# Kernel optimization log

Hardware: AMD Instinct MI355X
Metric: run time of the kernel (lower is better)

Reference implementation:

```python
import jax, jax.numpy as jnp
import numpy as np

# ExLoss constants (use_prior=False path)
T = 10.0
W_BU, W_H, W_TH = 1.0, 1.0, 3.0
P_MARGIN, N_MARGIN = 0.2, 0.3

B, C, D = 32, 40000, 2048


def setup_inputs() -> dict:
    key = jax.random.key(0)
    k1, k2, k3, k4 = jax.random.split(key, 4)
    inputs = jax.random.normal(k1, (B, D), dtype=jnp.float32)
    targets = jax.random.randint(k2, (B,), 0, 16)            # few identities -> positive pairs exist
    indexs = jax.random.randint(k3, (B,), 0, C)              # unused (use_prior=False)
    label_to_pairs = jnp.zeros((B,), dtype=jnp.int32)        # unused placeholder
    V = jax.random.normal(k4, (C, D), dtype=jnp.float32)
    V = V / jnp.linalg.norm(V, axis=1, keepdims=True)        # bank rows are L2-normalized by the EMA update
    return {"inputs": inputs, "V": V, "targets": targets,
            "label_to_pairs": label_to_pairs, "indexs": indexs}


def _masked_bce(logits, mask, target):
    # BCEWithLogits, reduction='mean' over masked elements; 0 if mask empty
    # per-elem: target*softplus(-x) + (1-target)*softplus(x)
    per = target * jax.nn.softplus(-logits) + (1.0 - target) * jax.nn.softplus(logits)
    cnt = jnp.sum(mask)
    s = jnp.sum(jnp.where(mask, per, 0.0))
    return jnp.where(cnt > 0, s / jnp.maximum(cnt, 1), 0.0)


def _ex_loss(inputs, V, targets):
    n = inputs.shape[0]
    # Exclusive: memory-bank matmul, scaled by t
    outputs = (inputs @ V.T) * T                                   # [B, C]
    # bu_loss: cross entropy (mean)
    logp = jax.nn.log_softmax(outputs, axis=1)
    bu_loss = -jnp.mean(jnp.take_along_axis(logp, targets[:, None], axis=1))

    # hard_negative_mining (batch sims, off-diagonal)
    ni = inputs / jnp.linalg.norm(inputs, axis=1, keepdims=True)
    sims = ni @ ni.T                                               # [B, B]
    eye = jnp.eye(n, dtype=bool)
    same = targets[:, None] == targets[None, :]
    pos = same & ~eye                                              # positive pairs, diag removed
    neg = ~same                                                    # negatives (diag is always 'same')
    # n_thrds: row min of psims BEFORE 2->-2 replacement (fill=2 where not positive)
    n_thrds = jnp.min(jnp.where(pos, sims, 2.0), axis=1, keepdims=True) - N_MARGIN
    # p_thrds: row max after 2->-2 replacement (fill=-2 where not positive)
    p_thrds = jnp.max(jnp.where(pos, sims, -2.0), axis=1, keepdims=True) - P_MARGIN
    hp_mask = pos & (sims < p_thrds)        # fill value 2 can never be < p_thrds (<= 0.8)
    hn_mask = neg & (sims > n_thrds)        # fill value -2 can never be > n_thrds
    h_loss = _masked_bce(sims, hp_mask, 1.0) + _masked_bce(sims, hn_mask, 0.0)

    # hard_negative_mining_with_table (only if no zero rows in V)
    active = jnp.all(jnp.sum(V, axis=1) != 0)
    nV = ni @ V.T                                                  # [B, C]
    n_th_t = jnp.take_along_axis(nV, targets[:, None], axis=1) - N_MARGIN  # [B,1]
    nsims_t = V[targets] @ V.T                                     # [B, C]
    t_mask = (n_th_t < nsims_t) & (nsims_t < 0.9999)
    th_loss = jnp.where(active, _masked_bce(nsims_t, t_mask, 0.0), 0.0)

    loss = W_BU * bu_loss + W_H * h_loss + W_TH * th_loss
    return loss, outputs


def reference(inputs, V, targets, label_to_pairs, indexs):
    # label_to_pairs / indexs unused: use_prior=False in ExLoss.__init__
    return _ex_loss(inputs, V, targets)
```

## Files before the change

### kernel.cpp

```cpp
#include <hip/hip_runtime.h>
#include <math.h>

#define B_ 32
#define C_ 40000
#define D_ 2048
#define T_SCALE 10.0f
#define P_MARG 0.2f
#define N_MARG 0.3f
#define NSTEP 64
#define KSPL 4
#define NCB 625
#define NBLK (NCB * KSPL)

typedef __attribute__((ext_vector_type(4))) float f32x4;
typedef __fp16 fp16x2 __attribute__((ext_vector_type(2)));
typedef _Float16 f16x2n __attribute__((ext_vector_type(2)));
typedef _Float16 half8_t __attribute__((ext_vector_type(8)));

#define OP1_OFF 0
#define OP_FLOATS (B_ * C_)
#define NS0_OFF (OP1_OFF + 3 * OP_FLOATS)
#define VR_OFF (NS0_OFF + 4 * OP_FLOATS)
#define VR_FLOATS C_
#define SC_OFF (VR_OFF + VR_FLOATS)
#define S_HLOSS 0
#define S_THSUM 1
#define S_THCNT 2
#define S_BAD 3
#define S_NTH 4
#define S_BU 36
#define SC_FLOATS 128
#define DT_OFF (SC_OFF + SC_FLOATS)
#define DT_FLOATS (32 * 32)
#define AF_OFF (DT_OFF + DT_FLOATS)
#define AF_FLOATS (NSTEP * 2048 / 2)
#define WS_FLOATS_TOTAL (AF_OFF + AF_FLOATS)

__device__ __forceinline__ float softplus_f(float x) {
    return (x > 0.f) ? (x + log1pf(expf(-x))) : log1pf(expf(x));
}

__device__ __forceinline__ unsigned pack_rtz(float x0, float x1) {
    fp16x2 h = __builtin_amdgcn_cvt_pkrtz(x0, x1);
    return __builtin_bit_cast(unsigned, h);
}

__device__ __forceinline__ unsigned pack_rtne(float x0, float x1) {
    f16x2n p = {(_Float16)x0, (_Float16)x1};
    return __builtin_bit_cast(unsigned, p);
}

__global__ __launch_bounds__(256) void build_Afrag(const float* __restrict__ in,
                                                   const float* __restrict__ V,
                                                   const int* __restrict__ tgt,
                                                   unsigned short* __restrict__ Af) {
    int s = blockIdx.x;
    int f = threadIdx.x >> 6;
    int l = threadIdx.x & 63;
    int row = f * 16 + (l & 15);
    int k = s * 32 + (l >> 4) * 8;
    const float* src = (row < 32) ? (in + (size_t)row * D_ + k)
                                  : (V + (size_t)tgt[row - 32] * D_ + k);
    f32x4 x0 = *(const f32x4*)src;
    f32x4 x1 = *(const f32x4*)(src + 4);
    uint4 u = make_uint4(pack_rtne(x0[0], x0[1]), pack_rtne(x0[2], x0[3]),
                         pack_rtne(x1[0], x1[1]), pack_rtne(x1[2], x1[3]));
    *(uint4*)(Af + (size_t)s * 2048 + (size_t)f * 512 + (size_t)l * 8) = u;
}

__global__ __launch_bounds__(256) void sims_dots(const float* __restrict__ in,
                                                 float* __restrict__ dt) {
    __shared__ float part[8][32];
    int i = blockIdx.x;
    int j = threadIdx.x & 31;
    int sl = threadIdx.x >> 5;
    const float4* a4 = (const float4*)(in + (size_t)i * D_ + sl * 256);
    const float4* b4 = (const float4*)(in + (size_t)j * D_ + sl * 256);
    float s = 0.f;
#pragma unroll 4
    for (int k = 0; k < 64; ++k) {
        float4 x = a4[k], y = b4[k];
        s += x.x * y.x + x.y * y.y + x.z * y.z + x.w * y.w;
    }
    part[sl][j] = s;
    __syncthreads();
    if (threadIdx.x < 32) {
        float t = 0.f;
#pragma unroll
        for (int p = 0; p < 8; ++p) t += part[p][threadIdx.x];
        dt[i * 32 + threadIdx.x] = t;
    }
}

__global__ __launch_bounds__(1024) void small_finish(const float* __restrict__ in,
                                                     const float* __restrict__ V,
                                                     const int* __restrict__ tgt,
                                                     float* __restrict__ ws) {
    __shared__ float sims[32][33];
    __shared__ float nthr[32], pthr[32];
    __shared__ int ts[32];
    __shared__ float diag[32];
    __shared__ float red[4];
    int tid = threadIdx.x;
    int i = tid >> 5, j = tid & 31;
    const float* dt = ws + DT_OFF;
    if (tid < 32) { ts[tid] = tgt[tid]; diag[tid] = dt[tid * 32 + tid]; }
    if (tid < 4) red[tid] = 0.f;
    __syncthreads();
    float sim = dt[i * 32 + j] * rsqrtf(diag[i] * diag[j]);
    sims[i][j] = sim;
    __syncthreads();
    if (tid < 32) {
        float nmin = 2.f, pmax = -2.f;
        int ti = ts[tid];
        for (int jj = 0; jj < 32; ++jj) {
            bool pos = (ts[jj] == ti) && (jj != tid);
            float v = sims[tid][jj];
            if (pos) { nmin = fminf(nmin, v); pmax = fmaxf(pmax, v); }
        }
        nthr[tid] = nmin - N_MARG;
        pthr[tid] = pmax - P_MARG;
    }
    __syncthreads();
    bool pos = (ts[i] == ts[j]) && (i != j);
    bool neg = (ts[i] != ts[j]);
    if (pos && sim < pthr[i]) { atomicAdd(&red[0], softplus_f(-sim)); atomicAdd(&red[1], 1.f); }
    if (neg && sim > nthr[i]) { atomicAdd(&red[2], softplus_f(sim)); atomicAdd(&red[3], 1.f); }

    const float4* a4 = (const float4*)(in + (size_t)i * D_);
    const float4* v4 = (const float4*)(V + (size_t)ts[i] * D_);
    float sn = 0.f;
    for (int k = j; k < D_ / 4; k += 32) {
        float4 x = a4[k], y = v4[k];
        sn += x.x * y.x + x.y * y.y + x.z * y.z + x.w * y.w;
    }
    for (int off = 16; off > 0; off >>= 1) sn += __shfl_down(sn, off, 32);
    if (j == 0) ws[SC_OFF + S_NTH + i] = sn * rsqrtf(diag[i]) - N_MARG;
    __syncthreads();
    if (tid == 0) {
        float h = 0.f;
        if (red[1] > 0.f) h += red[0] / red[1];
        if (red[3] > 0.f) h += red[2] / red[3];
        ws[SC_OFF + S_HLOSS] = h;
    }
}

__global__ __launch_bounds__(256, 2) void gemm_mfma(const float* __restrict__ V,
                                                    const unsigned short* __restrict__ Af,
                                                    float* __restrict__ op0,
                                                    float* __restrict__ ws) {
    const int l = threadIdx.x & 63;
    const int w = threadIdx.x >> 6;
    const int ks = blockIdx.x & 3;
    const int cb = blockIdx.x >> 2;
    const int col = l & 15, g = l >> 4;
    const int c = cb * 64 + w * 16 + col;

    const float* vp = V + (size_t)c * D_ + ks * 512 + g * 8;
    const unsigned short* ap = Af + (size_t)(ks * 16) * 2048 + (size_t)l * 8;

    f32x4 z = {0.f, 0.f, 0.f, 0.f};
    f32x4 acc0 = z, acc1 = z, acc2 = z, acc3 = z;
    float vsum = 0.f;

    uint4 Aa[4][4], Ab[4][4];
    f32x4 VaA[4], VbA[4], VaB[4], VbB[4];

#define LOADB(AB, VA, VB, t0)                                      \
    _Pragma("unroll") for (int s = 0; s < 4; ++s) {                \
        const unsigned short* as = ap + (size_t)((t0) + s) * 2048; \
        AB[s][0] = *(const uint4*)(as + 0 * 512);                  \
        AB[s][1] = *(const uint4*)(as + 1 * 512);                  \
        AB[s][2] = *(const uint4*)(as + 2 * 512);                  \
        AB[s][3] = *(const uint4*)(as + 3 * 512);                  \
        VA[s] = *(const f32x4*)(vp + ((t0) + s) * 32);             \
        VB[s] = *(const f32x4*)(vp + ((t0) + s) * 32 + 4);         \
    }

#define COMPB(AB, VA, VB)                                                          \
    _Pragma("unroll") for (int s = 0; s < 4; ++s) {                                \
        f32x4 v0 = VA[s], v1 = VB[s];                                              \
        vsum += v0[0] + v0[1] + v0[2] + v0[3] + v1[0] + v1[1] + v1[2] + v1[3];     \
        uint4 bu = make_uint4(pack_rtz(v0[0], v0[1]), pack_rtz(v0[2], v0[3]),      \
                              pack_rtz(v1[0], v1[1]), pack_rtz(v1[2], v1[3]));     \
        half8_t bh = __builtin_bit_cast(half8_t, bu);                              \
        half8_t A0h = __builtin_bit_cast(half8_t, AB[s][0]);                       \
        half8_t A1h = __builtin_bit_cast(half8_t, AB[s][1]);                       \
        half8_t A2h = __builtin_bit_cast(half8_t, AB[s][2]);                       \
        half8_t A3h = __builtin_bit_cast(half8_t, AB[s][3]);                       \
        acc0 = __builtin_amdgcn_mfma_f32_16x16x32_f16(A0h, bh, acc0, 0, 0, 0);     \
        acc1 = __builtin_amdgcn_mfma_f32_16x16x32_f16(A1h, bh, acc1, 0, 0, 0);     \
        acc2 = __builtin_amdgcn_mfma_f32_16x16x32_f16(A2h, bh, acc2, 0, 0, 0);     \
        acc3 = __builtin_amdgcn_mfma_f32_16x16x32_f16(A3h, bh, acc3, 0, 0, 0);     \
    }

    LOADB(Aa, VaA, VbA, 0);
    LOADB(Ab, VaB, VbB, 4);
    COMPB(Aa, VaA, VbA);
    LOADB(Aa, VaA, VbA, 8);
    COMPB(Ab, VaB, VbB);
    LOADB(Ab, VaB, VbB, 12);
    COMPB(Aa, VaA, VbA);
    COMPB(Ab, VaB, VbB);

#undef LOADB
#undef COMPB

    vsum += __shfl_xor(vsum, 16);
    vsum += __shfl_xor(vsum, 32);
    if (g == 0) atomicAdd(&ws[VR_OFF + c], vsum);

    float* op = (ks == 0) ? op0 : (ws + OP1_OFF + (size_t)(ks - 1) * OP_FLOATS);
    float* nsp = ws + NS0_OFF + (size_t)ks * OP_FLOATS;
#pragma unroll
    for (int r = 0; r < 4; ++r) {
        int rr = g * 4 + r;
        op[(size_t)rr * C_ + c] = acc0[r];
        op[(size_t)(16 + rr) * C_ + c] = acc1[r];
        nsp[(size_t)rr * C_ + c] = acc2[r];
        nsp[(size_t)(16 + rr) * C_ + c] = acc3[r];
    }
}

__global__ __launch_bounds__(1024) void lse_th_combine(float* __restrict__ out,
                                                       const int* __restrict__ tgt,
                                                       float* __restrict__ ws) {
    int b = blockIdx.x;
    int tid = threadIdx.x;
    __shared__ float sm[1024], ss[1024], sts[1024], stc[1024];
    __shared__ float xt;
    const float* p1 = ws + OP1_OFF + 0 * OP_FLOATS + (size_t)b * C_;
    const float* p2 = ws + OP1_OFF + 1 * OP_FLOATS + (size_t)b * C_;
    const float* p3 = ws + OP1_OFF + 2 * OP_FLOATS + (size_t)b * C_;
    const float* q0 = ws + NS0_OFF + 0 * OP_FLOATS + (size_t)b * C_;
    const float* q1 = ws + NS0_OFF + 1 * OP_FLOATS + (size_t)b * C_;
    const float* q2 = ws + NS0_OFF + 2 * OP_FLOATS + (size_t)b * C_;
    const float* q3 = ws + NS0_OFF + 3 * OP_FLOATS + (size_t)b * C_;
    float* orow = out + (size_t)b * C_;
    float nth = ws[SC_OFF + S_NTH + b];
    int tg = tgt[b];
    float m = -INFINITY, s = 0.f, ts = 0.f, tc = 0.f;
    for (int c = tid; c < C_; c += 1024) {
        float x = (orow[c] + p1[c] + p2[c] + p3[c]) * T_SCALE;
        orow[c] = x;
        if (c == tg) xt = x;
        float mn = fmaxf(m, x);
        s = s * expf(m - mn) + expf(x - mn);
        m = mn;
        float q = q0[c] + q1[c] + q2[c] + q3[c];
        if (q > nth && q < 0.9999f) { ts += softplus_f(q); tc += 1.f; }
    }
    sm[tid] = m; ss[tid] = s; sts[tid] = ts; stc[tid] = tc;
    __syncthreads();
    for (int st2 = 512; st2 > 0; st2 >>= 1) {
        if (tid < st2) {
            float m2 = sm[tid + st2], s2 = ss[tid + st2];
            float M = fmaxf(sm[tid], m2);
            ss[tid] = ss[tid] * expf(sm[tid] - M) + s2 * expf(m2 - M);
            sm[tid] = M;
            sts[tid] += sts[tid + st2];
            stc[tid] += stc[tid + st2];
        }
        __syncthreads();
    }
    if (tid == 0) {
        ws[SC_OFF + S_BU + b] = (sm[0] + logf(ss[0])) - xt;
        if (stc[0] != 0.f) {
            atomicAdd(&ws[SC_OFF + S_THSUM], sts[0]);
            atomicAdd(&ws[SC_OFF + S_THCNT], stc[0]);
        }
    }
}

__global__ __launch_bounds__(256) void vrow_check(const float* __restrict__ ws_c,
                                                  float* __restrict__ ws) {
    int c = blockIdx.x * 256 + threadIdx.x;
    if (c < C_ && ws_c[VR_OFF + c] == 0.0f) ws[SC_OFF + S_BAD] = 1.0f;
}

__global__ void finalize(const float* __restrict__ ws, float* __restrict__ out0) {
    if (threadIdx.x == 0 && blockIdx.x == 0) {
        float bu = 0.f;
        for (int b = 0; b < 32; ++b) bu += ws[SC_OFF + S_BU + b];
        bu /= 32.f;
        float h = ws[SC_OFF + S_HLOSS];
        float th = 0.f;
        float cnt = ws[SC_OFF + S_THCNT];
        if (ws[SC_OFF + S_BAD] == 0.f && cnt > 0.f) th = ws[SC_OFF + S_THSUM] / cnt;
        out0[0] = 1.0f * bu + 1.0f * h + 3.0f * th;
    }
}

extern "C" void kernel_launch(void* const* d_in, const int* in_sizes, int n_in,
                              void* d_out, int out_size, void* d_ws, size_t ws_size,
                              hipStream_t stream) {
    const float* in = (const float*)d_in[0];
    const float* V = (const float*)d_in[1];
    const int* tgt = (const int*)d_in[2];
    float* outp = (float*)d_out;
    float* ws = (float*)d_ws;
    unsigned short* Af = (unsigned short*)(ws + AF_OFF);

    (void)hipMemsetAsync((void*)(ws + VR_OFF), 0,
                         (size_t)(VR_FLOATS + SC_FLOATS) * sizeof(float), stream);

    build_Afrag<<<NSTEP, 256, 0, stream>>>(in, V, tgt, Af);
    sims_dots<<<32, 256, 0, stream>>>(in, ws + DT_OFF);
    small_finish<<<1, 1024, 0, stream>>>(in, V, tgt, ws);

    gemm_mfma<<<NBLK, 256, 0, stream>>>(V, Af, outp + 1, ws);

    lse_th_combine<<<B_, 1024, 0, stream>>>(outp + 1, tgt, ws);
    vrow_check<<<(C_ + 255) / 256, 256, 0, stream>>>(ws, ws);
    finalize<<<1, 64, 0, stream>>>(ws, outp);
}
```

Baseline: 220.9 us.

## Stage V tiles into LDS via global_load_lds with swizzled double buffering

The GEMM kernel now copies V rows into a double-buffered, XOR-swizzled shared-memory tile with direct global-to-LDS loads, so each row is fetched as contiguous 512-byte chunks rather than strided per-lane 32-byte reads. The A fragments are loaded straight from global memory inside the compute loop instead of being prefetched into registers. This is meant to improve coalescing of the dominant V stream and to cut register pressure. In exchange it adds 64KB of LDS per block and block-wide barriers, which may lower occupancy, and A-load latency is no longer hidden by explicit prefetch.

```diff
diff --git a/kernel.cpp b/kernel.cpp
--- a/kernel.cpp
+++ b/kernel.cpp
@@ -16,6 +16,11 @@
 typedef __fp16 fp16x2 __attribute__((ext_vector_type(2)));
 typedef _Float16 f16x2n __attribute__((ext_vector_type(2)));
 typedef _Float16 half8_t __attribute__((ext_vector_type(8)));
+
+#define GLL(gsrc, ldst)                                                          \
+    __builtin_amdgcn_global_load_lds(                                            \
+        (const __attribute__((address_space(1))) unsigned int*)(gsrc),           \
+        (__attribute__((address_space(3))) unsigned int*)(ldst), 16, 0, 0)
 
 #define OP1_OFF 0
 #define OP_FLOATS (B_ * C_)
@@ -149,62 +154,73 @@
                                                     const unsigned short* __restrict__ Af,
                                                     float* __restrict__ op0,
                                                     float* __restrict__ ws) {
+    __shared__ float Va[4][16][128];
+    __shared__ float Vb[4][16][128];
     const int l = threadIdx.x & 63;
     const int w = threadIdx.x >> 6;
     const int ks = blockIdx.x & 3;
     const int cb = blockIdx.x >> 2;
     const int col = l & 15, g = l >> 4;
-    const int c = cb * 64 + w * 16 + col;
-
-    const float* vp = V + (size_t)c * D_ + ks * 512 + g * 8;
-    const unsigned short* ap = Af + (size_t)(ks * 16) * 2048 + (size_t)l * 8;
+    const int crow0 = cb * 64 + w * 16;
+    const int c = crow0 + col;
+    const int lhi = l >> 5;
+    const int l31 = l & 31;
+    const int c7 = col & 7;
 
     f32x4 z = {0.f, 0.f, 0.f, 0.f};
     f32x4 acc0 = z, acc1 = z, acc2 = z, acc3 = z;
     float vsum = 0.f;
 
-    uint4 Aa[4][4], Ab[4][4];
-    f32x4 VaA[4], VbA[4], VaB[4], VbB[4];
-
-#define LOADB(AB, VA, VB, t0)                                      \
-    _Pragma("unroll") for (int s = 0; s < 4; ++s) {                \
-        const unsigned short* as = ap + (size_t)((t0) + s) * 2048; \
-        AB[s][0] = *(const uint4*)(as + 0 * 512);                  \
-        AB[s][1] = *(const uint4*)(as + 1 * 512);                  \
-        AB[s][2] = *(const uint4*)(as + 2 * 512);                  \
-        AB[s][3] = *(const uint4*)(as + 3 * 512);                  \
-        VA[s] = *(const f32x4*)(vp + ((t0) + s) * 32);             \
-        VB[s] = *(const f32x4*)(vp + ((t0) + s) * 32 + 4);         \
-    }
-
-#define COMPB(AB, VA, VB)                                                          \
+#define STAGE_V(VB, stg)                                                          \
+    do {                                                                          \
+        const size_t kb_ = (size_t)ks * 512 + (size_t)(stg) * 128;                \
+        _Pragma("unroll") for (int j = 0; j < 8; ++j) {                           \
+            const int r_ = 2 * j + lhi;                                           \
+            GLL(V + (size_t)(crow0 + r_) * D_ + kb_ + 4 * (l31 ^ (r_ & 7)),       \
+                &VB[w][2 * j][0]);                                                \
+        }                                                                         \
+    } while (0)
+
+#define COMPUTE(VB, stg)                                                           \
     _Pragma("unroll") for (int s = 0; s < 4; ++s) {                                \
-        f32x4 v0 = VA[s], v1 = VB[s];                                              \
+        const int sg = ks * 16 + (stg) * 4 + s;                                    \
+        const unsigned short* as_ = Af + (size_t)sg * 2048 + (size_t)l * 8;        \
+        uint4 a0 = *(const uint4*)(as_ + 0 * 512);                                 \
+        uint4 a1 = *(const uint4*)(as_ + 1 * 512);                                 \
+        uint4 a2 = *(const uint4*)(as_ + 2 * 512);                                 \
+        uint4 a3 = *(const uint4*)(as_ + 3 * 512);                                 \
+        const int cb0 = s * 8 + g * 2;                                             \
+        f32x4 v0 = *(const f32x4*)&VB[w][col][4 * (cb0 ^ c7)];                     \
+        f32x4 v1 = *(const f32x4*)&VB[w][col][4 * ((cb0 + 1) ^ c7)];               \
         vsum += v0[0] + v0[1] + v0[2] + v0[3] + v1[0] + v1[1] + v1[2] + v1[3];     \
         uint4 bu = make_uint4(pack_rtz(v0[0], v0[1]), pack_rtz(v0[2], v0[3]),      \
                               pack_rtz(v1[0], v1[1]), pack_rtz(v1[2], v1[3]));     \
         half8_t bh = __builtin_bit_cast(half8_t, bu);                              \
-        half8_t A0h = __builtin_bit_cast(half8_t, AB[s][0]);                       \
-        half8_t A1h = __builtin_bit_cast(half8_t, AB[s][1]);                       \
-        half8_t A2h = __builtin_bit_cast(half8_t, AB[s][2]);                       \
-        half8_t A3h = __builtin_bit_cast(half8_t, AB[s][3]);                       \
+        half8_t A0h = __builtin_bit_cast(half8_t, a0);                             \
+        half8_t A1h = __builtin_bit_cast(half8_t, a1);                             \
+        half8_t A2h = __builtin_bit_cast(half8_t, a2);                             \
+        half8_t A3h = __builtin_bit_cast(half8_t, a3);                             \
         acc0 = __builtin_amdgcn_mfma_f32_16x16x32_f16(A0h, bh, acc0, 0, 0, 0);     \
         acc1 = __builtin_amdgcn_mfma_f32_16x16x32_f16(A1h, bh, acc1, 0, 0, 0);     \
         acc2 = __builtin_amdgcn_mfma_f32_16x16x32_f16(A2h, bh, acc2, 0, 0, 0);     \
         acc3 = __builtin_amdgcn_mfma_f32_16x16x32_f16(A3h, bh, acc3, 0, 0, 0);     \
     }
 
-    LOADB(Aa, VaA, VbA, 0);
-    LOADB(Ab, VaB, VbB, 4);
-    COMPB(Aa, VaA, VbA);
-    LOADB(Aa, VaA, VbA, 8);
-    COMPB(Ab, VaB, VbB);
-    LOADB(Ab, VaB, VbB, 12);
-    COMPB(Aa, VaA, VbA);
-    COMPB(Ab, VaB, VbB);
-
-#undef LOADB
-#undef COMPB
+    STAGE_V(Va, 0);
+    __syncthreads();
+    STAGE_V(Vb, 1);
+    COMPUTE(Va, 0);
+    __syncthreads();
+    STAGE_V(Va, 2);
+    COMPUTE(Vb, 1);
+    __syncthreads();
+    STAGE_V(Vb, 3);
+    COMPUTE(Va, 2);
+    __syncthreads();
+    COMPUTE(Vb, 3);
+
+#undef STAGE_V
+#undef COMPUTE
 
     vsum += __shfl_xor(vsum, 16);
     vsum += __shfl_xor(vsum, 32);
```

Result: faster. 204.8 us (-7.3%).
